# Kernel optimization log

Hardware: AMD Instinct MI355X
Metric: run time of the kernel (lower is better)

The kernel has to match this reference:

```python
import jax, jax.numpy as jnp
import numpy as np

HEADS = 16
HEAD_DIM = 64
EMB = HEADS * HEAD_DIM
MAX_REL = 512
B, L = 4, 1024


def _rel_indices(length_q, length_k):
    # Shaw-style clipped relative distance indices into the embeddings table
    dist = jnp.arange(length_k)[None, :] - jnp.arange(length_q)[:, None]
    return jnp.clip(dist, -MAX_REL, MAX_REL) + MAX_REL  # [Lq, Lk] in [0, 2*MAX_REL]


def setup_inputs() -> dict:
    key = jax.random.key(0)
    ks = jax.random.split(key, 16)
    d = {
        "query": jax.random.normal(ks[0], (B, L, EMB), jnp.float32),
        "key": jax.random.normal(ks[1], (B, L, EMB), jnp.float32),
        "value": jax.random.normal(ks[2], (B, L, EMB), jnp.float32),
        "mask": jnp.ones((B, 1, L, L), jnp.int32),
        # per-head Linear(head_dims, head_dims) weights stored torch-style [out, in]
        "Wq": jax.random.normal(ks[3], (HEAD_DIM, HEAD_DIM), jnp.float32) / np.sqrt(HEAD_DIM),
        "bq": jax.random.normal(ks[4], (HEAD_DIM,), jnp.float32) * 0.02,
        "Wk": jax.random.normal(ks[5], (HEAD_DIM, HEAD_DIM), jnp.float32) / np.sqrt(HEAD_DIM),
        "bk": jax.random.normal(ks[6], (HEAD_DIM,), jnp.float32) * 0.02,
        "Wv": jax.random.normal(ks[7], (HEAD_DIM, HEAD_DIM), jnp.float32) / np.sqrt(HEAD_DIM),
        "bv": jax.random.normal(ks[8], (HEAD_DIM,), jnp.float32) * 0.02,
        "Wfc": jax.random.normal(ks[9], (EMB, EMB), jnp.float32) / np.sqrt(EMB),
        "bfc": jax.random.normal(ks[10], (EMB,), jnp.float32) * 0.02,
        "rel_k_table": jax.random.normal(ks[11], (2 * MAX_REL + 1, HEAD_DIM), jnp.float32) * 0.02,
        "rel_v_table": jax.random.normal(ks[12], (2 * MAX_REL + 1, HEAD_DIM), jnp.float32) * 0.02,
    }
    return d


def reference(query, key, value, mask, Wq, bq, Wk, bk, Wv, bv, Wfc, bfc, rel_k_table, rel_v_table):
    b, lq, _ = query.shape
    lk = key.shape[1]
    # split heads then per-head linear projections (torch Linear: x @ W.T + b)
    q = query.reshape(b, lq, HEADS, HEAD_DIM) @ Wq.T + bq
    k = key.reshape(b, lk, HEADS, HEAD_DIM) @ Wk.T + bk
    v = value.reshape(b, lk, HEADS, HEAD_DIM) @ Wv.T + bv

    score = jnp.einsum('bqhd,bkhd->bhqk', q, k)  # [B,H,Lq,Lk]
    score = jnp.where(mask == 0, jnp.float32(-1e20), score)

    idx = _rel_indices(lq, lk)
    a_key = rel_k_table[idx]    # [Lq, Lk, D]
    a_val = rel_v_table[idx]    # [Lq, Lk, D]
    score = score + jnp.einsum('blhd,lrd->bhlr', q, a_key)

    attn = jax.nn.softmax(score / np.sqrt(HEAD_DIM), axis=-1)

    out = jnp.einsum('bhqv,bvhd->bqhd', attn, v)
    # original: einsum('brhl,hld->bhrd', attn[b,h,q,k], a_val[q,k,d]) -> [b,q,h,d]
    out = out + jnp.einsum('bhql,qld->bqhd', attn, a_val)
    out = out.reshape(b, lq, EMB)
    return out @ Wfc.T + bfc
```

## Files before the change

kernel.cpp:

```cpp
#include <hip/hip_runtime.h>
#include <hip/hip_bf16.h>
#include <hip/hip_fp16.h>

#define SEQ 1024
#define HEADS 16
#define HDIM 64
#define EMB 1024
#define TQ 32
#define KQ 256
#define PBA_S 264
#define PBB_S 328
#define RELK_ROWS 1040
#define RELV_S 1064

typedef __bf16 bf16x8 __attribute__((ext_vector_type(8)));
typedef float floatx4 __attribute__((ext_vector_type(4)));
typedef unsigned short u16x4 __attribute__((ext_vector_type(4)));

#if __has_builtin(__builtin_amdgcn_exp2f)
#define EXP2F(x) __builtin_amdgcn_exp2f(x)
#else
#define EXP2F(x) exp2f(x)
#endif

#define QSCALE 0.18033688011112042f
#define PBIAS 6.0f

static __device__ __forceinline__ unsigned short f2bu(float f) {
    __bf16 h = (__bf16)f;
    return __builtin_bit_cast(unsigned short, h);
}
static __device__ __forceinline__ float b2f(unsigned short u) {
    unsigned v = ((unsigned)u) << 16;
    return __builtin_bit_cast(float, v);
}

#define NW (1024 * 1024)
#define NRK (RELK_ROWS * 64)
#define NRV (64 * RELV_S)
#define CONVB ((NW + NRK + NRV) / 256)
#define PREPY 1626
__global__ __launch_bounds__(256) void sa_projprep_kernel(
    const float* __restrict__ qin, const float* __restrict__ kin,
    const float* __restrict__ vin,
    const float* __restrict__ Wq, const float* __restrict__ Wk,
    const float* __restrict__ Wv,
    const float* __restrict__ bq, const float* __restrict__ bk,
    const float* __restrict__ bv_,
    const float* __restrict__ Wfc, const float* __restrict__ relk,
    const float* __restrict__ relv, const int* __restrict__ mask,
    unsigned short* __restrict__ qb, unsigned short* __restrict__ kb,
    unsigned short* __restrict__ vtb,
    unsigned short* __restrict__ wfcb, unsigned short* __restrict__ relkb,
    unsigned short* __restrict__ relvtb, unsigned* __restrict__ part) {
    __shared__ unsigned wok[4];
    const int t = threadIdx.x;
    const int which = blockIdx.y;
    const int bx = blockIdx.x;

    if (bx >= 1024) {
        const int gidx = (bx - 1024) + which * PREPY;
        if (gidx < CONVB) {
            int i = gidx * 256 + t;
            if (i < NW) {
                wfcb[i] = f2bu(Wfc[i]);
            } else if (i < NW + NRK) {
                int j = i - NW;
                int r = j >> 6, d = j & 63;
                relkb[j] = (r <= 1024) ? f2bu(relk[r * 64 + d]) : 0;
            } else {
                int j = i - NW - NRK;
                int d = j / RELV_S, c = j - d * RELV_S;
                relvtb[j] = (c <= 1024) ? f2bu(relv[c * 64 + d]) : 0;
            }
        } else if (gidx < CONVB + 256) {
            const int mb = gidx - CONVB;
            const int b = mb >> 6, chunk = mb & 63;
            const int4* p = (const int4*)(mask + (size_t)b * (SEQ * SEQ) + chunk * 16384);
            int ok = 1;
#pragma unroll
            for (int i = 0; i < 16; ++i) {
                int4 v = p[t + i * 256];
                ok &= (v.x != 0 && v.y != 0 && v.z != 0 && v.w != 0) ? 1 : 0;
            }
            unsigned long long bal = __ballot(ok);
            if ((t & 63) == 0) wok[t >> 6] = (bal == ~0ull) ? 1u : 0u;
            __syncthreads();
            if (t == 0)
                part[b * 64 + chunk] = (wok[0] & wok[1] & wok[2] & wok[3]) ? 0xFFFFFFFFu : 0u;
        }
        return;
    }

    const int w = t >> 6, lane = t & 63;
    const int quad = lane >> 4, l16 = lane & 15;
    const int r0 = (bx >> 2) * 16;
    const int h = (bx & 3) * 4 + w;
    const int bidx = r0 >> 10;
    const int l0 = r0 & 1023;
    const float* x = (which == 0) ? qin : (which == 1) ? kin : vin;
    const float* Wsrc = (which == 0) ? Wq : (which == 1) ? Wk : Wv;
    const float* bias = (which == 0) ? bq : (which == 1) ? bk : bv_;

    bf16x8 wf[4][2];
#pragma unroll
    for (int dt = 0; dt < 4; ++dt)
#pragma unroll
        for (int ks = 0; ks < 2; ++ks) {
            const float* wp = Wsrc + (size_t)(dt * 16 + l16) * 64 + ks * 32 + quad * 8;
            float4 lo = *(const float4*)wp;
            float4 hi = *(const float4*)(wp + 4);
            unsigned short pw[8];
            pw[0] = f2bu(lo.x); pw[1] = f2bu(lo.y); pw[2] = f2bu(lo.z); pw[3] = f2bu(lo.w);
            pw[4] = f2bu(hi.x); pw[5] = f2bu(hi.y); pw[6] = f2bu(hi.z); pw[7] = f2bu(hi.w);
            wf[dt][ks] = *(bf16x8*)pw;
        }

    bf16x8 xf[2];
#pragma unroll
    for (int ks = 0; ks < 2; ++ks) {
        const float* xp = x + (size_t)(r0 + l16) * EMB + h * 64 + ks * 32 + quad * 8;
        float4 lo = *(const float4*)xp;
        float4 hi = *(const float4*)(xp + 4);
        unsigned short px[8];
        px[0] = f2bu(lo.x); px[1] = f2bu(lo.y); px[2] = f2bu(lo.z); px[3] = f2bu(lo.w);
        px[4] = f2bu(hi.x); px[5] = f2bu(hi.y); px[6] = f2bu(hi.z); px[7] = f2bu(hi.w);
        xf[ks] = *(bf16x8*)px;
    }
    const int bh = bidx * HEADS + h;

    if (which < 2) {
        float biasd[4];
#pragma unroll
        for (int dt = 0; dt < 4; ++dt) biasd[dt] = bias[dt * 16 + l16];
        const float sc = (which == 0) ? QSCALE : 1.0f;
        unsigned short* dst = (which == 0) ? qb : kb;
        floatx4 acc[4];
#pragma unroll
        for (int dt = 0; dt < 4; ++dt) acc[dt] = floatx4{0.f, 0.f, 0.f, 0.f};
#pragma unroll
        for (int dt = 0; dt < 4; ++dt)
#pragma unroll
            for (int ks = 0; ks < 2; ++ks)
                acc[dt] = __builtin_amdgcn_mfma_f32_16x16x32_bf16(xf[ks], wf[dt][ks], acc[dt], 0, 0, 0);
#pragma unroll
        for (int dt = 0; dt < 4; ++dt)
#pragma unroll
            for (int i = 0; i < 4; ++i) {
                const int lr = l0 + quad * 4 + i;
                float val = (acc[dt][i] + biasd[dt]) * sc;
                dst[((size_t)bh * SEQ + lr) * 64 + dt * 16 + l16] = f2bu(val);
            }
    } else {
        float biasv[4][4];
#pragma unroll
        for (int dt = 0; dt < 4; ++dt)
#pragma unroll
            for (int i = 0; i < 4; ++i) biasv[dt][i] = bias[dt * 16 + quad * 4 + i];
        floatx4 acc[4];
#pragma unroll
        for (int dt = 0; dt < 4; ++dt) acc[dt] = floatx4{0.f, 0.f, 0.f, 0.f};
#pragma unroll
        for (int dt = 0; dt < 4; ++dt)
#pragma unroll
            for (int ks = 0; ks < 2; ++ks)
                acc[dt] = __builtin_amdgcn_mfma_f32_16x16x32_bf16(wf[dt][ks], xf[ks], acc[dt], 0, 0, 0);
#pragma unroll
        for (int dt = 0; dt < 4; ++dt)
#pragma unroll
            for (int i = 0; i < 4; ++i) {
                const int d = dt * 16 + quad * 4 + i;
                float val = acc[dt][i] + biasv[dt][i];
                vtb[((size_t)bh * 64 + d) * SEQ + l0 + l16] = f2bu(val);
            }
    }
}

__global__ __launch_bounds__(512, 8) void sa_attn_kernel(
    const unsigned short* __restrict__ qb, const unsigned short* __restrict__ kb,
    const unsigned short* __restrict__ vtb, const int* __restrict__ mask,
    const unsigned short* __restrict__ relkb, const unsigned short* __restrict__ relvtb,
    const unsigned* __restrict__ part, __half* __restrict__ Opart,
    float* __restrict__ ms) {
    __shared__ __align__(16) unsigned short PbA[TQ * PBA_S];
    __shared__ __align__(16) unsigned short PbB[TQ * PBB_S];
    __shared__ unsigned sflag;

    const int tid = threadIdx.x;
    const int w = tid >> 6, lane = tid & 63;
    const int quad = lane >> 4, l16 = lane & 15;
    const int bid = blockIdx.x;
    const int quarter = bid & 3;
    const int qt = (bid >> 2) & 31;
    const int bh = bid >> 7;
    const int q0 = qt * TQ;
    const int k0 = quarter * KQ;
    const int b = bh >> 4;

    if (tid < 64) {
        unsigned f = part[b * 64 + tid];
        unsigned long long bal = __ballot(f != 0u);
        if (tid == 0) sflag = (bal == ~0ull) ? 1u : 0u;
    }

    const bool clipped = (k0 - (q0 + 31) < -512) || (k0 + 255 - q0 > 512);
    const int cmin = min(512, max(-512, k0 - (q0 + 31))) + 512;
    const int cmax = min(512, max(-512, k0 + 255 - q0)) + 512;
    const int rsb = cmin & ~15;
    const int cb0 = cmin & ~7;

    bf16x8 aq[2][2];
#pragma unroll
    for (int rt = 0; rt < 2; ++rt) {
        const unsigned short* qrow = qb + ((size_t)bh * SEQ + q0 + rt * 16 + l16) * 64;
        aq[rt][0] = *(const bf16x8*)(qrow + quad * 8);
        aq[rt][1] = *(const bf16x8*)(qrow + 32 + quad * 8);
    }

    {
        const int ct_lo = cmin >> 4, ct_hi = cmax >> 4;
        for (int ct = ct_lo + w; ct <= ct_hi; ct += 8) {
            bf16x8 bf0 = *(const bf16x8*)(relkb + (size_t)(ct * 16 + l16) * 64 + quad * 8);
            bf16x8 bf1 = *(const bf16x8*)(relkb + (size_t)(ct * 16 + l16) * 64 + 32 + quad * 8);
            floatx4 r0 = {0.f, 0.f, 0.f, 0.f}, r1 = {0.f, 0.f, 0.f, 0.f};
            r0 = __builtin_amdgcn_mfma_f32_16x16x32_bf16(bf0, aq[0][0], r0, 0, 0, 0);
            r0 = __builtin_amdgcn_mfma_f32_16x16x32_bf16(bf1, aq[0][1], r0, 0, 0, 0);
            r1 = __builtin_amdgcn_mfma_f32_16x16x32_bf16(bf0, aq[1][0], r1, 0, 0, 0);
            r1 = __builtin_amdgcn_mfma_f32_16x16x32_bf16(bf1, aq[1][1], r1, 0, 0, 0);
            const int co = ct * 16 + quad * 4 - rsb;
            u16x4 p0, p1;
#pragma unroll
            for (int i = 0; i < 4; ++i) { p0[i] = f2bu(r0[i]); p1[i] = f2bu(r1[i]); }
            *(u16x4*)&PbB[(size_t)l16 * PBB_S + co] = p0;
            *(u16x4*)&PbB[(size_t)(16 + l16) * PBB_S + co] = p1;
        }
    }
    __syncthreads();
    const bool mfull = (sflag != 0u);

    const int kc = w;
    floatx4 acc[2][2];
#pragma unroll
    for (int rt = 0; rt < 2; ++rt)
#pragma unroll
        for (int tt = 0; tt < 2; ++tt) acc[rt][tt] = floatx4{0.f, 0.f, 0.f, 0.f};
#pragma unroll
    for (int tt = 0; tt < 2; ++tt) {
        const unsigned short* krow = kb + ((size_t)bh * SEQ + k0 + kc * 32 + tt * 16 + l16) * 64;
        bf16x8 kf0 = *(const bf16x8*)(krow + quad * 8);
        bf16x8 kf1 = *(const bf16x8*)(krow + 32 + quad * 8);
        acc[0][tt] = __builtin_amdgcn_mfma_f32_16x16x32_bf16(kf0, aq[0][0], acc[0][tt], 0, 0, 0);
        acc[0][tt] = __builtin_amdgcn_mfma_f32_16x16x32_bf16(kf1, aq[0][1], acc[0][tt], 0, 0, 0);
        acc[1][tt] = __builtin_amdgcn_mfma_f32_16x16x32_bf16(kf0, aq[1][0], acc[1][tt], 0, 0, 0);
        acc[1][tt] = __builtin_amdgcn_mfma_f32_16x16x32_bf16(kf1, aq[1][1], acc[1][tt], 0, 0, 0);
    }
    if (!clipped) {
#pragma unroll
        for (int rt = 0; rt < 2; ++rt) {
            const unsigned short* rsrow = &PbB[(size_t)(rt * 16 + l16) * PBB_S];
            const int cb = k0 + kc * 32 - (q0 + rt * 16 + l16) + 512 - rsb;
#pragma unroll
            for (int tt = 0; tt < 2; ++tt)
#pragma unroll
                for (int i = 0; i < 4; ++i)
                    acc[rt][tt][i] += b2f(rsrow[cb + tt * 16 + quad * 4 + i]);
        }
    } else {
#pragma unroll
        for (int rt = 0; rt < 2; ++rt) {
            const unsigned short* rsrow = &PbB[(size_t)(rt * 16 + l16) * PBB_S];
            const int cb = k0 + kc * 32 - (q0 + rt * 16 + l16) + 512;
#pragma unroll
            for (int tt = 0; tt < 2; ++tt)
#pragma unroll
                for (int i = 0; i < 4; ++i) {
                    const int c = cb + tt * 16 + quad * 4 + i;
                    const int r = min(1024, max(0, c));
                    acc[rt][tt][i] += b2f(rsrow[r - rsb]);
                }
        }
    }
    __syncthreads();

    for (int g = tid; g < TQ * (PBB_S / 8); g += 512) {
        int row = g / (PBB_S / 8), j = g - row * (PBB_S / 8);
        *(uint4*)&PbB[row * PBB_S + j * 8] = make_uint4(0u, 0u, 0u, 0u);
    }
    __syncthreads();

#pragma unroll
    for (int rt = 0; rt < 2; ++rt) {
        const int q = q0 + rt * 16 + l16;
        unsigned short* parow = &PbA[(size_t)(rt * 16 + l16) * PBA_S + kc * 32];
        unsigned short* pbrow = &PbB[(size_t)(rt * 16 + l16) * PBB_S];
        const int cbase = k0 + kc * 32 - q + 512;
        const int* mrow = mask + (size_t)b * (SEQ * SEQ) + (size_t)q * SEQ;
#pragma unroll
        for (int tt = 0; tt < 2; ++tt) {
            u16x4 pk;
            if (mfull) {
#pragma unroll
                for (int i = 0; i < 4; ++i)
                    pk[i] = f2bu(EXP2F(acc[rt][tt][i] - PBIAS));
            } else {
#pragma unroll
                for (int i = 0; i < 4; ++i) {
                    const int k = k0 + kc * 32 + tt * 16 + quad * 4 + i;
                    float s = (mrow[k] == 0) ? -1e20f : acc[rt][tt][i];
                    pk[i] = f2bu(EXP2F(s - PBIAS));
                }
            }
            *(u16x4*)(parow + tt * 16 + quad * 4) = pk;
            const int c0 = cbase + tt * 16 + quad * 4;
            if (!clipped) {
#pragma unroll
                for (int i = 0; i < 4; ++i) pbrow[c0 + i - cb0] = pk[i];
            } else {
#pragma unroll
                for (int i = 0; i < 4; ++i) {
                    const int c = c0 + i;
                    if ((unsigned)(c - 1) < 1023u) pbrow[c - cb0] = pk[i];
                }
            }
        }
    }
    __syncthreads();

    {
        const int rt = w & 1;
        const int dq = w >> 1;
        floatx4 accA = {0.f, 0.f, 0.f, 0.f};
        floatx4 accB = {0.f, 0.f, 0.f, 0.f};
        floatx4 accS = {0.f, 0.f, 0.f, 0.f};
        floatx4 accSI = {0.f, 0.f, 0.f, 0.f};
        unsigned short ob[8];
#pragma unroll
        for (int j = 0; j < 8; ++j) ob[j] = 0x3F80;
        const bf16x8 onesf = *(bf16x8*)ob;
        const unsigned short* vbase = vtb + ((size_t)bh * 64 + dq * 16 + l16) * SEQ + k0;
        const unsigned short* rbase = relvtb + (size_t)(dq * 16 + l16) * RELV_S;
#pragma unroll
        for (int it = 0; it < 8; ++it) {
            const int co = it * 32 + quad * 8;
            bf16x8 ap = *(const bf16x8*)&PbA[(size_t)(rt * 16 + l16) * PBA_S + co];
            bf16x8 bv = *(const bf16x8*)(vbase + co);
            accA = __builtin_amdgcn_mfma_f32_16x16x32_bf16(ap, bv, accA, 0, 0, 0);
            accS = __builtin_amdgcn_mfma_f32_16x16x32_bf16(ap, onesf, accS, 0, 0, 0);
        }
        const int nksB = ((cmax - cb0) >> 5) + 1;
        for (int ks = 0; ks < nksB; ++ks) {
            const int co = ks * 32 + quad * 8;
            bf16x8 ar = *(const bf16x8*)&PbB[(size_t)(rt * 16 + l16) * PBB_S + co];
            bf16x8 br = *(const bf16x8*)(rbase + cb0 + co);
            accB = __builtin_amdgcn_mfma_f32_16x16x32_bf16(ar, br, accB, 0, 0, 0);
            accSI = __builtin_amdgcn_mfma_f32_16x16x32_bf16(ar, onesf, accSI, 0, 0, 0);
        }
        const float rv0 = b2f(rbase[0]);
        const float rv1 = b2f(rbase[1024]);
#pragma unroll
        for (int i = 0; i < 4; ++i) {
            const int row = rt * 16 + quad * 4 + i;
            const int q = q0 + row;
            const float tail = accS[i] - accSI[i];
            const float lowS = (q >= k0 + 512) ? tail : 0.f;
            const float highS = (q <= k0 - 257) ? tail : 0.f;
            const int R = bh * SEQ + q;
            float val = accA[i] + accB[i] + lowS * rv0 + highS * rv1;
            Opart[((size_t)R * 4 + quarter) * 64 + dq * 16 + l16] = __float2half(val);
        }
        if (dq == 0 && l16 == 0) {
#pragma unroll
            for (int i = 0; i < 4; ++i) {
                const int row = rt * 16 + quad * 4 + i;
                ms[(size_t)(bh * SEQ + q0 + row) * 4 + quarter] = accS[i];
            }
        }
    }
}

__global__ __launch_bounds__(256) void sa_combine_kernel(
    const __half* __restrict__ Opart, const float* __restrict__ ms,
    unsigned short* __restrict__ aob) {
    const int tid = threadIdx.x;
    const int R = blockIdx.x * 4 + (tid >> 6);
    const int d = tid & 63;
    float4 dn = *(const float4*)&ms[(size_t)R * 4];
    const float inv = 1.f / (dn.x + dn.y + dn.z + dn.w);
    float val = 0.f;
#pragma unroll
    for (int j = 0; j < 4; ++j)
        val += __half2float(Opart[((size_t)R * 4 + j) * 64 + d]);
    val *= inv;
    const int bh = R >> 10, q = R & 1023, b = bh >> 4, h = bh & 15;
    aob[((size_t)b * SEQ + q) * EMB + h * 64 + d] = f2bu(val);
}

__global__ __launch_bounds__(256, 2) void sa_fc_kernel(
    const unsigned short* __restrict__ A, const unsigned short* __restrict__ W,
    const float* __restrict__ bias, float* __restrict__ out) {
    const int t = threadIdx.x;
    const int w = t >> 6, lane = t & 63;
    const int quad = lane >> 4, l16 = lane & 15;
    const int mw = blockIdx.x * 64 + (w & 1) * 32;
    const int nw = blockIdx.y * 256 + (w >> 1) * 128;

    floatx4 acc[2][8];
#pragma unroll
    for (int mt = 0; mt < 2; ++mt)
#pragma unroll
        for (int j = 0; j < 8; ++j) acc[mt][j] = floatx4{0.f, 0.f, 0.f, 0.f};
    float bj[8];
#pragma unroll
    for (int j = 0; j < 8; ++j) bj[j] = bias[nw + j * 16 + l16];

    for (int ks = 0; ks < 32; ++ks) {
        const int co = ks * 32 + quad * 8;
        bf16x8 af0 = *(const bf16x8*)(A + (size_t)(mw + l16) * EMB + co);
        bf16x8 af1 = *(const bf16x8*)(A + (size_t)(mw + 16 + l16) * EMB + co);
#pragma unroll
        for (int j = 0; j < 8; ++j) {
            bf16x8 bf = *(const bf16x8*)(W + (size_t)(nw + j * 16 + l16) * EMB + co);
            acc[0][j] = __builtin_amdgcn_mfma_f32_16x16x32_bf16(af0, bf, acc[0][j], 0, 0, 0);
            acc[1][j] = __builtin_amdgcn_mfma_f32_16x16x32_bf16(af1, bf, acc[1][j], 0, 0, 0);
        }
    }
#pragma unroll
    for (int mt = 0; mt < 2; ++mt)
#pragma unroll
        for (int j = 0; j < 8; ++j) {
            const int col = nw + j * 16 + l16;
#pragma unroll
            for (int i = 0; i < 4; ++i) {
                const size_t row = mw + mt * 16 + quad * 4 + i;
                out[row * EMB + col] = acc[mt][j][i] + bj[j];
            }
        }
}

extern "C" void kernel_launch(void* const* d_in, const int* in_sizes, int n_in,
                              void* d_out, int out_size, void* d_ws, size_t ws_size,
                              hipStream_t stream) {
    const float* query = (const float*)d_in[0];
    const float* key = (const float*)d_in[1];
    const float* value = (const float*)d_in[2];
    const int* mask = (const int*)d_in[3];
    const float* Wq = (const float*)d_in[4];
    const float* bq = (const float*)d_in[5];
    const float* Wk = (const float*)d_in[6];
    const float* bk = (const float*)d_in[7];
    const float* Wv = (const float*)d_in[8];
    const float* bv = (const float*)d_in[9];
    const float* Wfc = (const float*)d_in[10];
    const float* bfc = (const float*)d_in[11];
    const float* relk = (const float*)d_in[12];
    const float* relv = (const float*)d_in[13];
    float* out = (float*)d_out;

    char* base = (char*)d_ws;
    const size_t MB = (size_t)1 << 20;
    unsigned short* qb = (unsigned short*)(base + 0 * MB);
    unsigned short* aob = qb;
    unsigned short* kb = (unsigned short*)(base + 8 * MB);
    unsigned short* vtb = (unsigned short*)(base + 16 * MB);
    unsigned short* wfcb = (unsigned short*)(base + 24 * MB);
    unsigned short* relkb = (unsigned short*)(base + 26 * MB);
    unsigned short* relvtb = (unsigned short*)(base + 26 * MB + 163840);
    unsigned* part = (unsigned*)(base + 26 * MB + 327680);
    float* ms = (float*)(base + 27 * MB);
    __half* Opart = (__half*)(base + 29 * MB);

    sa_projprep_kernel<<<dim3(1024 + PREPY, 3), 256, 0, stream>>>(
        query, key, value, Wq, Wk, Wv, bq, bk, bv,
        Wfc, relk, relv, mask, qb, kb, vtb, wfcb, relkb, relvtb, part);
    sa_attn_kernel<<<64 * 32 * 4, 512, 0, stream>>>(
        qb, kb, vtb, mask, relkb, relvtb, part, Opart, ms);
    sa_combine_kernel<<<(4 * HEADS * SEQ) / 4, 256, 0, stream>>>(Opart, ms, aob);
    sa_fc_kernel<<<dim3(64, 4), 256, 0, stream>>>(aob, wfcb, bfc, out);
}
```

Measured before the change: 400.6 us.

## Widen attention key tile to half sequence with 1024-thread blocks

```diff
diff --git a/kernel.cpp b/kernel.cpp
--- a/kernel.cpp
+++ b/kernel.cpp
@@ -7,9 +7,9 @@
 #define HDIM 64
 #define EMB 1024
 #define TQ 32
-#define KQ 256
-#define PBA_S 264
-#define PBB_S 328
+#define KQ 512
+#define PBA_S 520
+#define PBB_S 584
 #define RELK_ROWS 1040
 #define RELV_S 1064
 
@@ -176,7 +176,7 @@
     }
 }
 
-__global__ __launch_bounds__(512, 8) void sa_attn_kernel(
+__global__ __launch_bounds__(1024, 8) void sa_attn_kernel(
     const unsigned short* __restrict__ qb, const unsigned short* __restrict__ kb,
     const unsigned short* __restrict__ vtb, const int* __restrict__ mask,
     const unsigned short* __restrict__ relkb, const unsigned short* __restrict__ relvtb,
@@ -190,11 +190,11 @@
     const int w = tid >> 6, lane = tid & 63;
     const int quad = lane >> 4, l16 = lane & 15;
     const int bid = blockIdx.x;
-    const int quarter = bid & 3;
-    const int qt = (bid >> 2) & 31;
-    const int bh = bid >> 7;
+    const int kh = bid & 1;
+    const int qt = (bid >> 1) & 31;
+    const int bh = bid >> 6;
     const int q0 = qt * TQ;
-    const int k0 = quarter * KQ;
+    const int k0 = kh * KQ;
     const int b = bh >> 4;
 
     if (tid < 64) {
@@ -203,11 +203,12 @@
         if (tid == 0) sflag = (bal == ~0ull) ? 1u : 0u;
     }
 
-    const bool clipped = (k0 - (q0 + 31) < -512) || (k0 + 255 - q0 > 512);
+    const bool clipped = (k0 - (q0 + 31) < -512) || (k0 + 511 - q0 > 512);
     const int cmin = min(512, max(-512, k0 - (q0 + 31))) + 512;
-    const int cmax = min(512, max(-512, k0 + 255 - q0)) + 512;
-    const int rsb = cmin & ~15;
-    const int cb0 = cmin & ~7;
+    const int cmax = min(512, max(-512, k0 + 511 - q0)) + 512;
+    const int BASE = cmin & ~15;
+    const int nksB = ((cmax - BASE) >> 5) + 1;
+    const bool interior = (cmin > 0) && (cmax < 1024);
 
     bf16x8 aq[2][2];
 #pragma unroll
@@ -219,7 +220,7 @@
 
     {
         const int ct_lo = cmin >> 4, ct_hi = cmax >> 4;
-        for (int ct = ct_lo + w; ct <= ct_hi; ct += 8) {
+        for (int ct = ct_lo + w; ct <= ct_hi; ct += 16) {
             bf16x8 bf0 = *(const bf16x8*)(relkb + (size_t)(ct * 16 + l16) * 64 + quad * 8);
             bf16x8 bf1 = *(const bf16x8*)(relkb + (size_t)(ct * 16 + l16) * 64 + 32 + quad * 8);
             floatx4 r0 = {0.f, 0.f, 0.f, 0.f}, r1 = {0.f, 0.f, 0.f, 0.f};
@@ -227,7 +228,7 @@
             r0 = __builtin_amdgcn_mfma_f32_16x16x32_bf16(bf1, aq[0][1], r0, 0, 0, 0);
             r1 = __builtin_amdgcn_mfma_f32_16x16x32_bf16(bf0, aq[1][0], r1, 0, 0, 0);
             r1 = __builtin_amdgcn_mfma_f32_16x16x32_bf16(bf1, aq[1][1], r1, 0, 0, 0);
-            const int co = ct * 16 + quad * 4 - rsb;
+            const int co = ct * 16 + quad * 4 - BASE;
             u16x4 p0, p1;
 #pragma unroll
             for (int i = 0; i < 4; ++i) { p0[i] = f2bu(r0[i]); p1[i] = f2bu(r1[i]); }
@@ -258,7 +259,7 @@
 #pragma unroll
         for (int rt = 0; rt < 2; ++rt) {
             const unsigned short* rsrow = &PbB[(size_t)(rt * 16 + l16) * PBB_S];
-            const int cb = k0 + kc * 32 - (q0 + rt * 16 + l16) + 512 - rsb;
+            const int cb = k0 + kc * 32 - (q0 + rt * 16 + l16) + 512 - BASE;
 #pragma unroll
             for (int tt = 0; tt < 2; ++tt)
 #pragma unroll
@@ -276,15 +277,9 @@
                 for (int i = 0; i < 4; ++i) {
                     const int c = cb + tt * 16 + quad * 4 + i;
                     const int r = min(1024, max(0, c));
-                    acc[rt][tt][i] += b2f(rsrow[r - rsb]);
+                    acc[rt][tt][i] += b2f(rsrow[r - BASE]);
                 }
         }
-    }
-    __syncthreads();
-
-    for (int g = tid; g < TQ * (PBB_S / 8); g += 512) {
-        int row = g / (PBB_S / 8), j = g - row * (PBB_S / 8);
-        *(uint4*)&PbB[row * PBB_S + j * 8] = make_uint4(0u, 0u, 0u, 0u);
     }
     __syncthreads();
 
@@ -314,21 +309,38 @@
             const int c0 = cbase + tt * 16 + quad * 4;
             if (!clipped) {
 #pragma unroll
-                for (int i = 0; i < 4; ++i) pbrow[c0 + i - cb0] = pk[i];
+                for (int i = 0; i < 4; ++i) pbrow[c0 + i - BASE] = pk[i];
             } else {
 #pragma unroll
                 for (int i = 0; i < 4; ++i) {
                     const int c = c0 + i;
-                    if ((unsigned)(c - 1) < 1023u) pbrow[c - cb0] = pk[i];
+                    if ((unsigned)(c - 1) < 1023u) pbrow[c - BASE] = pk[i];
                 }
             }
         }
     }
+    {
+        const int RE = BASE + nksB * 32;
+#pragma unroll
+        for (int rr = 0; rr < 2; ++rr) {
+            const int row = 2 * w + rr;
+            const int q = q0 + row;
+            const int crow0 = k0 + 512 - q;
+            int st_lo, st_hi1;
+            if (!clipped) { st_lo = crow0; st_hi1 = crow0 + 512; }
+            else { st_lo = max(crow0, 1); st_hi1 = max(st_lo, min(crow0 + 512, 1024)); }
+            unsigned short* pr = &PbB[(size_t)row * PBB_S];
+            for (int x = BASE + lane; x < st_lo; x += 64) pr[x - BASE] = 0;
+            for (int x = st_hi1 + lane; x < RE; x += 64) pr[x - BASE] = 0;
+        }
+    }
     __syncthreads();
 
     {
-        const int rt = w & 1;
-        const int dq = w >> 1;
+        const int rtF = w & 1;
+        const int dq = (w >> 1) & 3;
+        const int khr = w >> 3;
+        const int slot = kh * 2 + khr;
         floatx4 accA = {0.f, 0.f, 0.f, 0.f};
         floatx4 accB = {0.f, 0.f, 0.f, 0.f};
         floatx4 accS = {0.f, 0.f, 0.f, 0.f};
@@ -337,42 +349,72 @@
 #pragma unroll
         for (int j = 0; j < 8; ++j) ob[j] = 0x3F80;
         const bf16x8 onesf = *(bf16x8*)ob;
-        const unsigned short* vbase = vtb + ((size_t)bh * 64 + dq * 16 + l16) * SEQ + k0;
+        const unsigned short* vbase = vtb + ((size_t)bh * 64 + dq * 16 + l16) * SEQ + k0 + khr * 256;
         const unsigned short* rbase = relvtb + (size_t)(dq * 16 + l16) * RELV_S;
-#pragma unroll
-        for (int it = 0; it < 8; ++it) {
-            const int co = it * 32 + quad * 8;
-            bf16x8 ap = *(const bf16x8*)&PbA[(size_t)(rt * 16 + l16) * PBA_S + co];
-            bf16x8 bv = *(const bf16x8*)(vbase + co);
-            accA = __builtin_amdgcn_mfma_f32_16x16x32_bf16(ap, bv, accA, 0, 0, 0);
-            accS = __builtin_amdgcn_mfma_f32_16x16x32_bf16(ap, onesf, accS, 0, 0, 0);
-        }
-        const int nksB = ((cmax - cb0) >> 5) + 1;
-        for (int ks = 0; ks < nksB; ++ks) {
-            const int co = ks * 32 + quad * 8;
-            bf16x8 ar = *(const bf16x8*)&PbB[(size_t)(rt * 16 + l16) * PBB_S + co];
-            bf16x8 br = *(const bf16x8*)(rbase + cb0 + co);
-            accB = __builtin_amdgcn_mfma_f32_16x16x32_bf16(ar, br, accB, 0, 0, 0);
-            accSI = __builtin_amdgcn_mfma_f32_16x16x32_bf16(ar, onesf, accSI, 0, 0, 0);
+        const unsigned short* parowF = &PbA[(size_t)(rtF * 16 + l16) * PBA_S + khr * 256];
+        const unsigned short* pbrowF = &PbB[(size_t)(rtF * 16 + l16) * PBB_S];
+        const int ksLo = khr ? 9 : 0;
+        const int ksHi = khr ? nksB : min(nksB, 9);
+        if (interior) {
+            if (dq == 0) {
+#pragma unroll
+                for (int it = 0; it < 8; ++it) {
+                    const int co = it * 32 + quad * 8;
+                    bf16x8 ap = *(const bf16x8*)(parowF + co);
+                    bf16x8 bv = *(const bf16x8*)(vbase + co);
+                    accA = __builtin_amdgcn_mfma_f32_16x16x32_bf16(ap, bv, accA, 0, 0, 0);
+                    accS = __builtin_amdgcn_mfma_f32_16x16x32_bf16(ap, onesf, accS, 0, 0, 0);
+                }
+            } else {
+#pragma unroll
+                for (int it = 0; it < 8; ++it) {
+                    const int co = it * 32 + quad * 8;
+                    bf16x8 ap = *(const bf16x8*)(parowF + co);
+                    bf16x8 bv = *(const bf16x8*)(vbase + co);
+                    accA = __builtin_amdgcn_mfma_f32_16x16x32_bf16(ap, bv, accA, 0, 0, 0);
+                }
+            }
+            for (int ks = ksLo; ks < ksHi; ++ks) {
+                const int co = ks * 32 + quad * 8;
+                bf16x8 ar = *(const bf16x8*)(pbrowF + co);
+                bf16x8 br = *(const bf16x8*)(rbase + BASE + co);
+                accB = __builtin_amdgcn_mfma_f32_16x16x32_bf16(ar, br, accB, 0, 0, 0);
+            }
+        } else {
+#pragma unroll
+            for (int it = 0; it < 8; ++it) {
+                const int co = it * 32 + quad * 8;
+                bf16x8 ap = *(const bf16x8*)(parowF + co);
+                bf16x8 bv = *(const bf16x8*)(vbase + co);
+                accA = __builtin_amdgcn_mfma_f32_16x16x32_bf16(ap, bv, accA, 0, 0, 0);
+                accS = __builtin_amdgcn_mfma_f32_16x16x32_bf16(ap, onesf, accS, 0, 0, 0);
+            }
+            for (int ks = ksLo; ks < ksHi; ++ks) {
+                const int co = ks * 32 + quad * 8;
+                bf16x8 ar = *(const bf16x8*)(pbrowF + co);
+                bf16x8 br = *(const bf16x8*)(rbase + BASE + co);
+                accB = __builtin_amdgcn_mfma_f32_16x16x32_bf16(ar, br, accB, 0, 0, 0);
+                accSI = __builtin_amdgcn_mfma_f32_16x16x32_bf16(ar, onesf, accSI, 0, 0, 0);
+            }
         }
         const float rv0 = b2f(rbase[0]);
         const float rv1 = b2f(rbase[1024]);
 #pragma unroll
         for (int i = 0; i < 4; ++i) {
-            const int row = rt * 16 + quad * 4 + i;
+            const int row = rtF * 16 + quad * 4 + i;
             const int q = q0 + row;
-            const float tail = accS[i] - accSI[i];
+            const float tail = interior ? 0.f : (accS[i] - accSI[i]);
             const float lowS = (q >= k0 + 512) ? tail : 0.f;
-            const float highS = (q <= k0 - 257) ? tail : 0.f;
+            const float highS = (q <= k0 - 1) ? tail : 0.f;
             const int R = bh * SEQ + q;
             float val = accA[i] + accB[i] + lowS * rv0 + highS * rv1;
-            Opart[((size_t)R * 4 + quarter) * 64 + dq * 16 + l16] = __float2half(val);
+            Opart[((size_t)R * 4 + slot) * 64 + dq * 16 + l16] = __float2half(val);
         }
         if (dq == 0 && l16 == 0) {
 #pragma unroll
             for (int i = 0; i < 4; ++i) {
-                const int row = rt * 16 + quad * 4 + i;
-                ms[(size_t)(bh * SEQ + q0 + row) * 4 + quarter] = accS[i];
+                const int row = rtF * 16 + quad * 4 + i;
+                ms[(size_t)(bh * SEQ + q0 + row) * 4 + slot] = accS[i];
             }
         }
     }
@@ -472,7 +514,7 @@
     sa_projprep_kernel<<<dim3(1024 + PREPY, 3), 256, 0, stream>>>(
         query, key, value, Wq, Wk, Wv, bq, bk, bv,
         Wfc, relk, relv, mask, qb, kb, vtb, wfcb, relkb, relvtb, part);
-    sa_attn_kernel<<<64 * 32 * 4, 512, 0, stream>>>(
+    sa_attn_kernel<<<64 * 32 * 2, 1024, 0, stream>>>(
         qb, kb, vtb, mask, relkb, relvtb, part, Opart, ms);
     sa_combine_kernel<<<(4 * HEADS * SEQ) / 4, 256, 0, stream>>>(Opart, ms, aob);
     sa_fc_kernel<<<dim3(64, 4), 256, 0, stream>>>(aob, wfcb, bfc, out);
```

Result: slower. 412.1 us (+2.9%).
